# Kernel tuning notes

Hardware: AMD Instinct MI355X
Metric: run time of the kernel (lower is better)

Reference implementation:

```python
import jax, jax.numpy as jnp
import numpy as np

NCE_T = 0.07
TOP_K_RATIO = 0.5
BOTTOM_K_RATIO = 0.1


def setup_inputs() -> dict:
    key = jax.random.key(0)
    k1, k2 = jax.random.split(key)
    N, D = 8192, 256
    feat_q = jax.random.normal(k1, (N, D), dtype=jnp.float32)
    feat_k = jax.random.normal(k2, (N, D), dtype=jnp.float32)
    return {"feat_q": feat_q, "feat_k": feat_k}


def reference(feat_q, feat_k):
    # 2D path of RankNCELoss.forward: feat_q, feat_k are [N, D]
    N = feat_q.shape[0]
    feat_k = jax.lax.stop_gradient(feat_k)  # feat_k.detach()

    # l_pos: per-row dot product  [N, 1]
    l_pos = jnp.sum(feat_q * feat_k, axis=-1, keepdims=True)

    # full similarity matrix [N, N]
    sim = feat_q @ feat_k.T

    # mask diagonal (positives) with -inf
    eye = jnp.eye(N, dtype=bool)
    sim_masked = jnp.where(eye, -jnp.inf, sim)

    # descending sort per row (negate + ascending argsort)
    order = jnp.argsort(-sim_masked, axis=1)               # sorted_indices
    sorted_sim = jnp.take_along_axis(sim_masked, order, axis=1)

    num_neg = N - 1
    k_top = max(1, int(num_neg * TOP_K_RATIO))
    k_bottom = max(0, int(num_neg * BOTTOM_K_RATIO))

    ranks = jnp.arange(N)
    rank_ok = (ranks >= k_bottom) & (ranks < k_top)        # [N]
    select_mask = rank_ok[None, :] & (sorted_sim > -jnp.inf)

    vals = jnp.where(select_mask, sorted_sim, jnp.float32(-10.0))
    rows = jnp.arange(N)[:, None]
    l_neg = jnp.full((N, N), -10.0, dtype=feat_q.dtype).at[rows, order].set(vals)

    out = jnp.concatenate([l_pos, l_neg], axis=1) / NCE_T  # [N, N+1]
    # CrossEntropyLoss(reduction='none') with target 0
    loss = -jax.nn.log_softmax(out, axis=-1)[:, 0]
    return loss
```

## Files before the change

### kernel.cpp

```cpp
#include <hip/hip_runtime.h>
#include <hip/hip_bf16.h>

#define NROW 8192
#define NDIM 256
#define INV_T (1.0f / 0.07f)
#define K_BOT 819
#define K_TOP 4095
#define N_SEL 3276
#define N_UNSEL 4916

typedef unsigned int u32;
typedef unsigned short u16;
typedef short s16;
typedef unsigned long long u64;
typedef __bf16 bf16_t;
typedef s16 s16x8 __attribute__((ext_vector_type(8)));
typedef float f32x4 __attribute__((ext_vector_type(4)));

__device__ __forceinline__ u16 bfbits(float f) {
    return __builtin_bit_cast(u16, (bf16_t)f);
}
__device__ __forceinline__ u16 map16(u16 b) {
    return (b & 0x8000u) ? (u16)~b : (u16)(b | 0x8000u);
}
__device__ __forceinline__ float unmap16(u32 m) {
    u16 b = (m & 0x8000u) ? (u16)(m & 0x7FFFu) : (u16)~(u16)m;
    return __uint_as_float(((u32)b) << 16);
}

__device__ __forceinline__ void gload16(const void* g, void* l) {
    __builtin_amdgcn_global_load_lds(
        (const __attribute__((address_space(1))) u32*)g,
        (__attribute__((address_space(3))) u32*)l, 16, 0, 0);
}

__global__ __launch_bounds__(256) void cvt_bf16(const float* __restrict__ in0,
                                                const float* __restrict__ in1,
                                                u16* __restrict__ out0,
                                                u16* __restrict__ out1) {
    int b = blockIdx.x;
    const float* in = (b < 2048) ? in0 : in1;
    u16* out = (b < 2048) ? out0 : out1;
    int i = ((b & 2047) * 256 + threadIdx.x) * 4;
    float4 v = *(const float4*)(in + i);
    ushort4 o;
    o.x = bfbits(v.x); o.y = bfbits(v.y); o.z = bfbits(v.z); o.w = bfbits(v.w);
    *(ushort4*)(out + i) = o;
}

__global__ __launch_bounds__(512) void gemm_keys(const u16* __restrict__ Qb,
                                                 const u16* __restrict__ Kb,
                                                 u16* __restrict__ Cp) {
    constexpr int BK = 64;
    __shared__ __align__(16) char smem[128 * 132 * 2];
    u16* sA = (u16*)smem;
    u16* sB = (u16*)(smem + 128 * BK * 2);
    u16* sC = (u16*)smem;

    const int tid  = threadIdx.x;
    const int lane = tid & 63;
    const int wid  = tid >> 6;
    const int wr = wid & 1;
    const int wc = wid >> 1;
    const int bm = blockIdx.y * 128;
    const int bn = blockIdx.x * 128;
    const int kg = lane >> 4;
    const int fr = lane & 15;

    const int srr = lane >> 3;
    const int srj = (lane & 7) ^ srr;

    f32x4 acc[4][2] = {};

    for (int k0 = 0; k0 < NDIM; k0 += BK) {
        __syncthreads();
#pragma unroll
        for (int s = 0; s < 2; ++s) {
            int seg = wid * 2 + s;
            int row = seg * 8 + srr;
            gload16(Qb + (size_t)(bm + row) * NDIM + k0 + srj * 8, &sA[seg * 512]);
            gload16(Kb + (size_t)(bn + row) * NDIM + k0 + srj * 8, &sB[seg * 512]);
        }
        __syncthreads();

#pragma unroll
        for (int kk = 0; kk < 2; ++kk) {
            s16x8 af[4], bfv[2];
            const int jp = (kk * 4 + kg) ^ (fr & 7);
#pragma unroll
            for (int m = 0; m < 4; ++m) {
                int row = wr * 64 + m * 16 + fr;
                af[m] = *(const s16x8*)(&sA[row * BK + jp * 8]);
            }
#pragma unroll
            for (int n = 0; n < 2; ++n) {
                int row = wc * 32 + n * 16 + fr;
                bfv[n] = *(const s16x8*)(&sB[row * BK + jp * 8]);
            }
#pragma unroll
            for (int m = 0; m < 4; ++m)
#pragma unroll
                for (int n = 0; n < 2; ++n)
                    acc[m][n] = __builtin_amdgcn_mfma_f32_16x16x32_bf16(
                        af[m], bfv[n], acc[m][n], 0, 0, 0);
        }
    }

    __syncthreads();
#pragma unroll
    for (int m = 0; m < 4; ++m)
#pragma unroll
        for (int n = 0; n < 2; ++n)
#pragma unroll
            for (int jj = 0; jj < 4; ++jj) {
                int r = wr * 64 + m * 16 + kg * 4 + jj;
                int c = wc * 32 + n * 16 + fr;
                sC[r * 132 + c] = map16(bfbits(acc[m][n][jj]));
            }
    __syncthreads();
    if (bm == bn) {
        if (tid < 128) sC[tid * 132 + tid] = 0;
        __syncthreads();
    }
#pragma unroll
    for (int it = 0; it < 4; ++it) {
        int idx = it * 512 + tid;
        int row = idx >> 4, col8 = (idx & 15) * 8;
        *(uint4*)(&Cp[(size_t)(bm + row) * NROW + bn + col8]) =
            *(const uint4*)(&sC[row * 132 + col8]);
    }
}

__device__ __forceinline__ u32 wave_sum_u32(u32 x) {
#pragma unroll
    for (int o = 32; o; o >>= 1) x += __shfl_down(x, o);
    return __shfl(x, 0);
}

__device__ __forceinline__ void resolve_slot(const u32* sub, int slot, u32 rem,
                                             int lane, u32* idxOut, u32* gtOut) {
    u32 word = sub[slot * 64 + lane];
    u32 c0 = word & 0xFFFFu, c1 = word >> 16;
    u32 s0 = c0 + c1, suf = s0;
#pragma unroll
    for (int o = 1; o < 64; o <<= 1) {
        u32 v = __shfl_down(suf, o);
        if (lane + o < 64) suf += v;
    }
    u32 TexL = suf - s0;
    u32 f = 0, pk = 0;
    u32 ab0 = TexL + c1;
    if (rem >= ab0 && rem < ab0 + c0) { f = 1; pk = ((u32)(lane * 2) << 16) | ab0; }
    if (rem >= TexL && rem < TexL + c1) { f = 1; pk = ((u32)(lane * 2 + 1) << 16) | TexL; }
    u64 mm = __ballot(f != 0);
    pk = __shfl(pk, (int)(__ffsll((unsigned long long)mm) - 1));
    *idxOut = pk >> 16;
    *gtOut = pk & 0xFFFFu;
}

__device__ u32 bisect_row(const uint4* rp, u32 rank, int lane) {
    u32 lo = 0, hi = 65535;
    while (lo < hi) {
        u32 mid = (lo + hi) >> 1;
        u32 pc = 0;
        for (int i = 0; i < 16; ++i) {
            uint4 v = rp[i * 64 + lane];
            pc += (u32)((v.x & 0xFFFFu) > mid) + (u32)((v.x >> 16) > mid)
                + (u32)((v.y & 0xFFFFu) > mid) + (u32)((v.y >> 16) > mid)
                + (u32)((v.z & 0xFFFFu) > mid) + (u32)((v.z >> 16) > mid)
                + (u32)((v.w & 0xFFFFu) > mid) + (u32)((v.w >> 16) > mid);
        }
        u32 c = wave_sum_u32(pc);
        if (c <= rank) hi = mid; else lo = mid + 1;
    }
    return lo;
}

#define KLO 0xC100u
#define KHI 0xC280u
#define RSPAN 0x180u
#define NSLOT 3

__global__ __launch_bounds__(128, 8) void rank_lse(const u16* __restrict__ Cp,
                                                   const float* __restrict__ fq,
                                                   const float* __restrict__ fk,
                                                   float* __restrict__ loss) {
    __shared__ u32 lds_s[2][NSLOT * 64];
    const int t = threadIdx.x;
    const int w = t >> 6;
    const int lane = t & 63;
    const int row = blockIdx.x * 2 + w;

    u32* sub = lds_s[w];
    const uint4* rp = (const uint4*)(Cp + (size_t)row * NROW);

    if (lane < 48) *(uint4*)&sub[lane * 4] = make_uint4(0, 0, 0, 0);

    float lp;
    {
        float4 q4 = *(const float4*)(fq + (size_t)row * NDIM + lane * 4);
        float4 k4 = *(const float4*)(fk + (size_t)row * NDIM + lane * 4);
        float p = q4.x * k4.x + q4.y * k4.y + q4.z * k4.z + q4.w * k4.w;
#pragma unroll
        for (int o = 32; o; o >>= 1) p += __shfl_down(p, o);
        lp = __shfl(p, 0);
    }

    u32 cntHi = 0;
#pragma unroll 4
    for (int i = 0; i < 16; ++i) {
        uint4 v = rp[i * 64 + lane];
        u32 vv[4] = { v.x, v.y, v.z, v.w };
#pragma unroll
        for (int q = 0; q < 4; ++q) {
#pragma unroll
            for (int hh = 0; hh < 2; ++hh) {
                u32 key = hh ? (vv[q] >> 16) : (vv[q] & 0xFFFFu);
                cntHi += (key >= KHI) ? 1u : 0u;
                u32 d = key - KLO;
                if (d < RSPAN)
                    atomicAdd(&sub[(d >> 7) * 64 + ((key >> 1) & 63u)],
                              (key & 1u) ? 0x10000u : 1u);
            }
        }
    }
    const u32 CH = wave_sum_u32(cntHi);

    u32 T0, T1, T2;
    {
        u32 w0 = sub[lane], w1 = sub[64 + lane], w2 = sub[128 + lane];
        u32 m0 = (w0 & 0xFFFFu) + (w0 >> 16);
        u32 m1 = (w1 & 0xFFFFu) + (w1 >> 16);
        u32 m2 = (w2 & 0xFFFFu) + (w2 >> 16);
        u32 p01 = wave_sum_u32(m0 | (m1 << 16));
        T2 = wave_sum_u32(m2);
        T0 = p01 & 0xFFFFu; T1 = p01 >> 16;
    }
    const u32 NR = T0 + T1 + T2;

    bool fb = !((CH <= (u32)K_BOT) && ((u32)K_BOT < CH + NR))
            || ((u32)(K_TOP - 1) < CH + NR);

    u32 ua = 0, Ga = 0, Ea = 0;
    float a = 0.f;
    int sA = 0;
    if (!fb) {
        const u32 AT2 = CH, AT1 = CH + T2, AT0 = AT1 + T1;
        u32 ATA;
        if ((u32)K_BOT >= AT0)      { sA = 0; ATA = AT0; }
        else if ((u32)K_BOT >= AT1) { sA = 1; ATA = AT1; }
        else                        { sA = 2; ATA = AT2; }
        const u32 remA = (u32)K_BOT - ATA;
        u32 idxA, gtA;
        resolve_slot(sub, sA, remA, lane, &idxA, &gtA);
        ua = KLO + ((u32)sA << 7) + idxA;
        Ga = ATA + gtA;
        {
            u32 wv = sub[sA * 64 + (idxA >> 1)];
            Ea = (idxA & 1u) ? (wv >> 16) : (wv & 0xFFFFu);
        }
        a = unmap16(ua);
        if (!(a >= 10.9f)) fb = true;
    }

    if (!fb) {
        const float m_ = fmaxf(fmaxf(lp, a), -10.0f) * INV_T;
        float sm = 0.f;
#pragma unroll
        for (int s = 0; s < NSLOT; ++s) {
            u32 wv = sub[s * 64 + lane];
            u32 c0 = wv & 0xFFFFu, c1 = wv >> 16;
            u32 k0 = KLO + ((u32)s << 7) + (u32)(lane * 2);
            u32 k1 = k0 | 1u;
            if (c0 && k0 < ua) sm += (float)c0 * __expf(unmap16(k0) * INV_T - m_);
            if (c1 && k1 < ua) sm += (float)c1 * __expf(unmap16(k1) * INV_T - m_);
        }
#pragma unroll
        for (int o = 32; o; o >>= 1) sm += __shfl_down(sm, o);
        if (lane == 0) {
            float expA = __expf(a * INV_T - m_);
            float tot = sm + (float)(int)(Ga + Ea - (u32)K_BOT) * expA;
            tot += __expf(lp * INV_T - m_)
                 + (float)N_UNSEL * __expf(-10.0f * INV_T - m_);
            loss[row] = m_ + __logf(tot) - lp * INV_T;
        }
    } else {
        u32 fua = bisect_row(rp, (u32)K_BOT, lane);
        u32 fub = bisect_row(rp, (u32)(K_TOP - 1), lane);
        float fa = unmap16(fua);
        const float m_ = fmaxf(fmaxf(lp, fa), -10.0f) * INV_T;
        u32 cga = 0, cea = 0, cgb = 0;
        float sm = 0.f;
        for (int i = 0; i < 16; ++i) {
            uint4 v = rp[i * 64 + lane];
            u32 vv[4] = { v.x, v.y, v.z, v.w };
#pragma unroll
            for (int q = 0; q < 4; ++q) {
#pragma unroll
                for (int hh = 0; hh < 2; ++hh) {
                    u32 u = hh ? (vv[q] >> 16) : (vv[q] & 0xFFFFu);
                    cga += (u > fua); cea += (u == fua); cgb += (u > fub);
                    if (u > fub && u < fua)
                        sm += __expf(unmap16(u) * INV_T - m_);
                }
            }
        }
        u32 fGa = wave_sum_u32(cga), fEa = wave_sum_u32(cea), fGb = wave_sum_u32(cgb);
#pragma unroll
        for (int o = 32; o; o >>= 1) sm += __shfl_down(sm, o);
        if (lane == 0) {
            float bv = unmap16(fub);
            float expA = __expf(fa * INV_T - m_);
            float tot;
            if (fua == fub) {
                tot = (float)N_SEL * expA;
            } else {
                float expB = __expf(bv * INV_T - m_);
                tot = sm + (float)(int)(fGa + fEa - (u32)K_BOT) * expA
                         + (float)(int)((u32)K_TOP - fGb) * expB;
            }
            tot += __expf(lp * INV_T - m_)
                 + (float)N_UNSEL * __expf(-10.0f * INV_T - m_);
            loss[row] = m_ + __logf(tot) - lp * INV_T;
        }
    }
}

extern "C" void kernel_launch(void* const* d_in, const int* in_sizes, int n_in,
                              void* d_out, int out_size, void* d_ws, size_t ws_size,
                              hipStream_t stream) {
    const float* fq = (const float*)d_in[0];
    const float* fk = (const float*)d_in[1];
    float* out = (float*)d_out;

    char* ws = (char*)d_ws;
    u16* keys = (u16*)ws;
    u16* qb = (u16*)(ws + (size_t)NROW * NROW * 2);
    u16* kb = qb + (size_t)NROW * NDIM;

    cvt_bf16<<<4096, 256, 0, stream>>>(fq, fk, qb, kb);
    gemm_keys<<<dim3(NROW / 128, NROW / 128), 512, 0, stream>>>(qb, kb, keys);
    rank_lse<<<NROW / 2, 128, 0, stream>>>(keys, fq, fk, out);
}
```

Measured before the change: 95.97 us.

## Fuse similarity GEMM with per-row histogram ranking, add fallback fixup kernel

```diff
diff --git a/kernel.cpp b/kernel.cpp
--- a/kernel.cpp
+++ b/kernel.cpp
@@ -8,6 +8,9 @@
 #define K_TOP 4095
 #define N_SEL 3276
 #define N_UNSEL 4916
+#define KLO 0xC100u
+#define KHI 0xC280u
+#define RSPAN 0x180u
 
 typedef unsigned int u32;
 typedef unsigned short u16;
@@ -27,11 +30,41 @@
     u16 b = (m & 0x8000u) ? (u16)(m & 0x7FFFu) : (u16)~(u16)m;
     return __uint_as_float(((u32)b) << 16);
 }
+__device__ __forceinline__ float bf2f(s16 v) {
+    return __uint_as_float(((u32)(u16)v) << 16);
+}
 
 __device__ __forceinline__ void gload16(const void* g, void* l) {
     __builtin_amdgcn_global_load_lds(
         (const __attribute__((address_space(1))) u32*)g,
         (__attribute__((address_space(3))) u32*)l, 16, 0, 0);
+}
+
+__device__ __forceinline__ u32 wave_sum_u32(u32 x) {
+#pragma unroll
+    for (int o = 32; o; o >>= 1) x += __shfl_down(x, o);
+    return __shfl(x, 0);
+}
+
+__device__ __forceinline__ void resolve_slot(const u32* sub, int slot, u32 rem,
+                                             int lane, u32* idxOut, u32* gtOut) {
+    u32 word = sub[slot * 64 + lane];
+    u32 c0 = word & 0xFFFFu, c1 = word >> 16;
+    u32 s0 = c0 + c1, suf = s0;
+#pragma unroll
+    for (int o = 1; o < 64; o <<= 1) {
+        u32 v = __shfl_down(suf, o);
+        if (lane + o < 64) suf += v;
+    }
+    u32 TexL = suf - s0;
+    u32 f = 0, pk = 0;
+    u32 ab0 = TexL + c1;
+    if (rem >= ab0 && rem < ab0 + c0) { f = 1; pk = ((u32)(lane * 2) << 16) | ab0; }
+    if (rem >= TexL && rem < TexL + c1) { f = 1; pk = ((u32)(lane * 2 + 1) << 16) | TexL; }
+    u64 mm = __ballot(f != 0);
+    pk = __shfl(pk, (int)(__ffsll((unsigned long long)mm) - 1));
+    *idxOut = pk >> 16;
+    *gtOut = pk & 0xFFFFu;
 }
 
 __global__ __launch_bounds__(256) void cvt_bf16(const float* __restrict__ in0,
@@ -48,276 +81,257 @@
     *(ushort4*)(out + i) = o;
 }
 
-__global__ __launch_bounds__(512) void gemm_keys(const u16* __restrict__ Qb,
-                                                 const u16* __restrict__ Kb,
-                                                 u16* __restrict__ Cp) {
-    constexpr int BK = 64;
-    __shared__ __align__(16) char smem[128 * 132 * 2];
-    u16* sA = (u16*)smem;
-    u16* sB = (u16*)(smem + 128 * BK * 2);
-    u16* sC = (u16*)smem;
+__global__ __launch_bounds__(512) void fused_rank(const u16* __restrict__ Qb,
+                                                  const u16* __restrict__ Kb,
+                                                  const float* __restrict__ fq,
+                                                  const float* __restrict__ fk,
+                                                  float* __restrict__ loss,
+                                                  u32* __restrict__ flags) {
+    __shared__ __align__(16) u16 sA[32 * 256];
+    __shared__ __align__(16) u16 sB[2][128 * 128];
+    __shared__ u32 hist[32 * 192];
+    __shared__ u32 cntHiRow[32];
 
     const int tid  = threadIdx.x;
     const int lane = tid & 63;
     const int wid  = tid >> 6;
-    const int wr = wid & 1;
-    const int wc = wid >> 1;
-    const int bm = blockIdx.y * 128;
-    const int bn = blockIdx.x * 128;
-    const int kg = lane >> 4;
-    const int fr = lane & 15;
-
-    const int srr = lane >> 3;
-    const int srj = (lane & 7) ^ srr;
-
-    f32x4 acc[4][2] = {};
-
-    for (int k0 = 0; k0 < NDIM; k0 += BK) {
+    const int kg   = lane >> 4;
+    const int fr   = lane & 15;
+    const int r0   = blockIdx.x * 32;
+
+    for (int i = tid; i < 32 * 192; i += 512) hist[i] = 0;
+    if (tid < 32) cntHiRow[tid] = 0;
+
+#pragma unroll
+    for (int s = 0; s < 2; ++s) {
+        int seg = wid * 2 + s;
+        int c = seg * 64 + lane;
+        int row = c >> 5, jp = c & 31;
+        int j = jp ^ (row & 7);
+        gload16(Qb + (size_t)(r0 + row) * NDIM + j * 8, &sA[seg * 512]);
+    }
+
+    auto STAGE = [&](int buf, int step) {
+        int h2 = step & 1, ct2 = step >> 1;
+        u16* dst = &sB[buf][0];
+#pragma unroll
+        for (int s2 = 0; s2 < 4; ++s2) {
+            int seg = wid * 4 + s2;
+            int c = seg * 64 + lane;
+            int row = c >> 4, jp = c & 15;
+            int j = jp ^ (row & 7);
+            gload16(Kb + (size_t)(ct2 * 128 + row) * NDIM + h2 * 128 + j * 8,
+                    dst + seg * 512);
+        }
+    };
+
+    STAGE(0, 0);
+    __syncthreads();
+
+    f32x4 acc[2] = {};
+    u32 cntHi[2][4] = {};
+
+    for (int s = 0; s < 128; ++s) {
+        const int buf = s & 1;
+        if (s + 1 < 128) STAGE(buf ^ 1, s + 1);
+        const int h = s & 1, ct = s >> 1;
+#pragma unroll
+        for (int ks = 0; ks < 4; ++ks) {
+            s16x8 bv = *(const s16x8*)&sB[buf][(wid * 16 + fr) * 128 +
+                                              (((ks * 4 + kg) ^ (fr & 7)) * 8)];
+#pragma unroll
+            for (int m = 0; m < 2; ++m) {
+                s16x8 av = *(const s16x8*)&sA[(m * 16 + fr) * 256 +
+                                              (((h * 16 + ks * 4 + kg) ^ (fr & 7)) * 8)];
+                acc[m] = __builtin_amdgcn_mfma_f32_16x16x32_bf16(av, bv, acc[m], 0, 0, 0);
+            }
+        }
+        if (h == 1) {
+            const int gcol = ct * 128 + wid * 16 + fr;
+#pragma unroll
+            for (int m = 0; m < 2; ++m) {
+#pragma unroll
+                for (int jj = 0; jj < 4; ++jj) {
+                    int rowLocal = m * 16 + kg * 4 + jj;
+                    u32 key = (u32)map16(bfbits(acc[m][jj]));
+                    if (r0 + rowLocal != gcol) {
+                        cntHi[m][jj] += (key >= KHI) ? 1u : 0u;
+                        u32 d = key - KLO;
+                        if (d < RSPAN)
+                            atomicAdd(&hist[rowLocal * 192 + (int)(d >> 7) * 64 +
+                                            (int)((key >> 1) & 63u)],
+                                      (key & 1u) ? 0x10000u : 1u);
+                    }
+                }
+                acc[m][0] = 0.f; acc[m][1] = 0.f; acc[m][2] = 0.f; acc[m][3] = 0.f;
+            }
+        }
         __syncthreads();
-#pragma unroll
-        for (int s = 0; s < 2; ++s) {
-            int seg = wid * 2 + s;
-            int row = seg * 8 + srr;
-            gload16(Qb + (size_t)(bm + row) * NDIM + k0 + srj * 8, &sA[seg * 512]);
-            gload16(Kb + (size_t)(bn + row) * NDIM + k0 + srj * 8, &sB[seg * 512]);
-        }
-        __syncthreads();
-
-#pragma unroll
-        for (int kk = 0; kk < 2; ++kk) {
-            s16x8 af[4], bfv[2];
-            const int jp = (kk * 4 + kg) ^ (fr & 7);
-#pragma unroll
-            for (int m = 0; m < 4; ++m) {
-                int row = wr * 64 + m * 16 + fr;
-                af[m] = *(const s16x8*)(&sA[row * BK + jp * 8]);
-            }
-#pragma unroll
-            for (int n = 0; n < 2; ++n) {
-                int row = wc * 32 + n * 16 + fr;
-                bfv[n] = *(const s16x8*)(&sB[row * BK + jp * 8]);
-            }
-#pragma unroll
-            for (int m = 0; m < 4; ++m)
-#pragma unroll
-                for (int n = 0; n < 2; ++n)
-                    acc[m][n] = __builtin_amdgcn_mfma_f32_16x16x32_bf16(
-                        af[m], bfv[n], acc[m][n], 0, 0, 0);
-        }
-    }
-
+    }
+
+#pragma unroll
+    for (int m = 0; m < 2; ++m)
+#pragma unroll
+        for (int jj = 0; jj < 4; ++jj) {
+            u32 v = cntHi[m][jj];
+            v += __shfl_down(v, 8, 16);
+            v += __shfl_down(v, 4, 16);
+            v += __shfl_down(v, 2, 16);
+            v += __shfl_down(v, 1, 16);
+            if (fr == 0) atomicAdd(&cntHiRow[m * 16 + kg * 4 + jj], v);
+        }
     __syncthreads();
-#pragma unroll
-    for (int m = 0; m < 4; ++m)
-#pragma unroll
-        for (int n = 0; n < 2; ++n)
-#pragma unroll
-            for (int jj = 0; jj < 4; ++jj) {
-                int r = wr * 64 + m * 16 + kg * 4 + jj;
-                int c = wc * 32 + n * 16 + fr;
-                sC[r * 132 + c] = map16(bfbits(acc[m][n][jj]));
-            }
-    __syncthreads();
-    if (bm == bn) {
-        if (tid < 128) sC[tid * 132 + tid] = 0;
-        __syncthreads();
-    }
-#pragma unroll
-    for (int it = 0; it < 4; ++it) {
-        int idx = it * 512 + tid;
-        int row = idx >> 4, col8 = (idx & 15) * 8;
-        *(uint4*)(&Cp[(size_t)(bm + row) * NROW + bn + col8]) =
-            *(const uint4*)(&sC[row * 132 + col8]);
-    }
-}
-
-__device__ __forceinline__ u32 wave_sum_u32(u32 x) {
-#pragma unroll
-    for (int o = 32; o; o >>= 1) x += __shfl_down(x, o);
-    return __shfl(x, 0);
-}
-
-__device__ __forceinline__ void resolve_slot(const u32* sub, int slot, u32 rem,
-                                             int lane, u32* idxOut, u32* gtOut) {
-    u32 word = sub[slot * 64 + lane];
-    u32 c0 = word & 0xFFFFu, c1 = word >> 16;
-    u32 s0 = c0 + c1, suf = s0;
-#pragma unroll
-    for (int o = 1; o < 64; o <<= 1) {
-        u32 v = __shfl_down(suf, o);
-        if (lane + o < 64) suf += v;
-    }
-    u32 TexL = suf - s0;
-    u32 f = 0, pk = 0;
-    u32 ab0 = TexL + c1;
-    if (rem >= ab0 && rem < ab0 + c0) { f = 1; pk = ((u32)(lane * 2) << 16) | ab0; }
-    if (rem >= TexL && rem < TexL + c1) { f = 1; pk = ((u32)(lane * 2 + 1) << 16) | TexL; }
-    u64 mm = __ballot(f != 0);
-    pk = __shfl(pk, (int)(__ffsll((unsigned long long)mm) - 1));
-    *idxOut = pk >> 16;
-    *gtOut = pk & 0xFFFFu;
-}
-
-__device__ u32 bisect_row(const uint4* rp, u32 rank, int lane) {
-    u32 lo = 0, hi = 65535;
-    while (lo < hi) {
-        u32 mid = (lo + hi) >> 1;
-        u32 pc = 0;
-        for (int i = 0; i < 16; ++i) {
-            uint4 v = rp[i * 64 + lane];
-            pc += (u32)((v.x & 0xFFFFu) > mid) + (u32)((v.x >> 16) > mid)
-                + (u32)((v.y & 0xFFFFu) > mid) + (u32)((v.y >> 16) > mid)
-                + (u32)((v.z & 0xFFFFu) > mid) + (u32)((v.z >> 16) > mid)
-                + (u32)((v.w & 0xFFFFu) > mid) + (u32)((v.w >> 16) > mid);
-        }
-        u32 c = wave_sum_u32(pc);
-        if (c <= rank) hi = mid; else lo = mid + 1;
-    }
-    return lo;
-}
-
-#define KLO 0xC100u
-#define KHI 0xC280u
-#define RSPAN 0x180u
-#define NSLOT 3
-
-__global__ __launch_bounds__(128, 8) void rank_lse(const u16* __restrict__ Cp,
-                                                   const float* __restrict__ fq,
-                                                   const float* __restrict__ fk,
-                                                   float* __restrict__ loss) {
-    __shared__ u32 lds_s[2][NSLOT * 64];
-    const int t = threadIdx.x;
-    const int w = t >> 6;
-    const int lane = t & 63;
-    const int row = blockIdx.x * 2 + w;
-
-    u32* sub = lds_s[w];
-    const uint4* rp = (const uint4*)(Cp + (size_t)row * NROW);
-
-    if (lane < 48) *(uint4*)&sub[lane * 4] = make_uint4(0, 0, 0, 0);
-
-    float lp;
-    {
-        float4 q4 = *(const float4*)(fq + (size_t)row * NDIM + lane * 4);
-        float4 k4 = *(const float4*)(fk + (size_t)row * NDIM + lane * 4);
-        float p = q4.x * k4.x + q4.y * k4.y + q4.z * k4.z + q4.w * k4.w;
-#pragma unroll
-        for (int o = 32; o; o >>= 1) p += __shfl_down(p, o);
-        lp = __shfl(p, 0);
-    }
-
-    u32 cntHi = 0;
-#pragma unroll 4
-    for (int i = 0; i < 16; ++i) {
-        uint4 v = rp[i * 64 + lane];
-        u32 vv[4] = { v.x, v.y, v.z, v.w };
-#pragma unroll
-        for (int q = 0; q < 4; ++q) {
-#pragma unroll
-            for (int hh = 0; hh < 2; ++hh) {
-                u32 key = hh ? (vv[q] >> 16) : (vv[q] & 0xFFFFu);
-                cntHi += (key >= KHI) ? 1u : 0u;
-                u32 d = key - KLO;
-                if (d < RSPAN)
-                    atomicAdd(&sub[(d >> 7) * 64 + ((key >> 1) & 63u)],
-                              (key & 1u) ? 0x10000u : 1u);
-            }
-        }
-    }
-    const u32 CH = wave_sum_u32(cntHi);
-
-    u32 T0, T1, T2;
-    {
-        u32 w0 = sub[lane], w1 = sub[64 + lane], w2 = sub[128 + lane];
-        u32 m0 = (w0 & 0xFFFFu) + (w0 >> 16);
-        u32 m1 = (w1 & 0xFFFFu) + (w1 >> 16);
-        u32 m2 = (w2 & 0xFFFFu) + (w2 >> 16);
-        u32 p01 = wave_sum_u32(m0 | (m1 << 16));
-        T2 = wave_sum_u32(m2);
-        T0 = p01 & 0xFFFFu; T1 = p01 >> 16;
-    }
-    const u32 NR = T0 + T1 + T2;
-
-    bool fb = !((CH <= (u32)K_BOT) && ((u32)K_BOT < CH + NR))
-            || ((u32)(K_TOP - 1) < CH + NR);
-
-    u32 ua = 0, Ga = 0, Ea = 0;
-    float a = 0.f;
-    int sA = 0;
-    if (!fb) {
-        const u32 AT2 = CH, AT1 = CH + T2, AT0 = AT1 + T1;
-        u32 ATA;
-        if ((u32)K_BOT >= AT0)      { sA = 0; ATA = AT0; }
-        else if ((u32)K_BOT >= AT1) { sA = 1; ATA = AT1; }
-        else                        { sA = 2; ATA = AT2; }
-        const u32 remA = (u32)K_BOT - ATA;
-        u32 idxA, gtA;
-        resolve_slot(sub, sA, remA, lane, &idxA, &gtA);
-        ua = KLO + ((u32)sA << 7) + idxA;
-        Ga = ATA + gtA;
+
+    for (int rr = 0; rr < 4; ++rr) {
+        const int rowLocal = rr * 8 + wid;
+        const int grow = r0 + rowLocal;
+        const u32* sub = &hist[rowLocal * 192];
+
+        float lp;
         {
-            u32 wv = sub[sA * 64 + (idxA >> 1)];
-            Ea = (idxA & 1u) ? (wv >> 16) : (wv & 0xFFFFu);
-        }
-        a = unmap16(ua);
-        if (!(a >= 10.9f)) fb = true;
-    }
-
-    if (!fb) {
+            float4 q4 = *(const float4*)(fq + (size_t)grow * NDIM + lane * 4);
+            float4 k4 = *(const float4*)(fk + (size_t)grow * NDIM + lane * 4);
+            float p = q4.x * k4.x + q4.y * k4.y + q4.z * k4.z + q4.w * k4.w;
+#pragma unroll
+            for (int o = 32; o; o >>= 1) p += __shfl_down(p, o);
+            lp = __shfl(p, 0);
+        }
+        const u32 CH = cntHiRow[rowLocal];
+
+        u32 T0, T1, T2;
+        {
+            u32 w0 = sub[lane], w1 = sub[64 + lane], w2 = sub[128 + lane];
+            u32 m0 = (w0 & 0xFFFFu) + (w0 >> 16);
+            u32 m1 = (w1 & 0xFFFFu) + (w1 >> 16);
+            u32 m2 = (w2 & 0xFFFFu) + (w2 >> 16);
+            u32 p01 = wave_sum_u32(m0 | (m1 << 16));
+            T2 = wave_sum_u32(m2);
+            T0 = p01 & 0xFFFFu; T1 = p01 >> 16;
+        }
+        const u32 NR = T0 + T1 + T2;
+
+        bool fb = !((CH <= (u32)K_BOT) && ((u32)K_BOT < CH + NR))
+                || ((u32)(K_TOP - 1) < CH + NR);
+
+        u32 ua = 0, Ga = 0, Ea = 0;
+        float a = 0.f;
+        if (!fb) {
+            const u32 AT2 = CH, AT1 = CH + T2, AT0 = AT1 + T1;
+            int sA_;
+            u32 ATA;
+            if ((u32)K_BOT >= AT0)      { sA_ = 0; ATA = AT0; }
+            else if ((u32)K_BOT >= AT1) { sA_ = 1; ATA = AT1; }
+            else                        { sA_ = 2; ATA = AT2; }
+            const u32 remA = (u32)K_BOT - ATA;
+            u32 idxA, gtA;
+            resolve_slot(sub, sA_, remA, lane, &idxA, &gtA);
+            ua = KLO + ((u32)sA_ << 7) + idxA;
+            Ga = ATA + gtA;
+            {
+                u32 wv = sub[sA_ * 64 + (idxA >> 1)];
+                Ea = (idxA & 1u) ? (wv >> 16) : (wv & 0xFFFFu);
+            }
+            a = unmap16(ua);
+            if (!(a >= 10.9f)) fb = true;
+        }
+
+        if (!fb) {
+            const float m_ = fmaxf(fmaxf(lp, a), -10.0f) * INV_T;
+            float sm = 0.f;
+#pragma unroll
+            for (int ss = 0; ss < 3; ++ss) {
+                u32 wv = sub[ss * 64 + lane];
+                u32 c0 = wv & 0xFFFFu, c1 = wv >> 16;
+                u32 k0 = KLO + ((u32)ss << 7) + (u32)(lane * 2);
+                u32 k1 = k0 | 1u;
+                if (c0 && k0 < ua) sm += (float)c0 * __expf(unmap16(k0) * INV_T - m_);
+                if (c1 && k1 < ua) sm += (float)c1 * __expf(unmap16(k1) * INV_T - m_);
+            }
+#pragma unroll
+            for (int o = 32; o; o >>= 1) sm += __shfl_down(sm, o);
+            if (lane == 0) {
+                float expA = __expf(a * INV_T - m_);
+                float tot = sm + (float)(int)(Ga + Ea - (u32)K_BOT) * expA;
+                tot += __expf(lp * INV_T - m_)
+                     + (float)N_UNSEL * __expf(-10.0f * INV_T - m_);
+                loss[grow] = m_ + __logf(tot) - lp * INV_T;
+                flags[grow] = 0u;
+            }
+        } else {
+            if (lane == 0) flags[grow] = 1u;
+        }
+    }
+}
+
+__global__ __launch_bounds__(256) void fixup(const u16* __restrict__ Qb,
+                                             const u16* __restrict__ Kb,
+                                             const float* __restrict__ fq,
+                                             const float* __restrict__ fk,
+                                             const u32* __restrict__ flags,
+                                             float* __restrict__ loss) {
+    __shared__ u16 skey[4][NROW];
+    const int wid = threadIdx.x >> 6, lane = threadIdx.x & 63;
+    const int gw = blockIdx.x * 4 + wid;
+
+    for (int rr = 0; rr < 32; ++rr) {
+        const int row = gw * 32 + rr;
+        if (!flags[row]) continue;
+        u16* K = skey[wid];
+        for (int j = 0; j < 128; ++j) {
+            int c = j * 64 + lane;
+            float dot = 0.f;
+            for (int kc = 0; kc < 32; ++kc) {
+                s16x8 qv = *(const s16x8*)(Qb + (size_t)row * NDIM + kc * 8);
+                s16x8 kv = *(const s16x8*)(Kb + (size_t)c * NDIM + kc * 8);
+#pragma unroll
+                for (int e = 0; e < 8; ++e) dot += bf2f(qv[e]) * bf2f(kv[e]);
+            }
+            K[c] = (c == row) ? (u16)0 : map16(bfbits(dot));
+        }
+        auto cntAbove = [&](u32 mid) {
+            u32 pc = 0;
+            for (int i = 0; i < 128; ++i) pc += (u32)(K[i * 64 + lane] > mid);
+            return wave_sum_u32(pc);
+        };
+        u32 lo = 0, hi = 65535;
+        while (lo < hi) { u32 mid = (lo + hi) >> 1;
+            if (cntAbove(mid) <= (u32)K_BOT) hi = mid; else lo = mid + 1; }
+        const u32 ua = lo;
+        lo = 0; hi = 65535;
+        while (lo < hi) { u32 mid = (lo + hi) >> 1;
+            if (cntAbove(mid) <= (u32)(K_TOP - 1)) hi = mid; else lo = mid + 1; }
+        const u32 ub = lo;
+        float lp;
+        {
+            float4 q4 = *(const float4*)(fq + (size_t)row * NDIM + lane * 4);
+            float4 k4 = *(const float4*)(fk + (size_t)row * NDIM + lane * 4);
+            float p = q4.x * k4.x + q4.y * k4.y + q4.z * k4.z + q4.w * k4.w;
+#pragma unroll
+            for (int o = 32; o; o >>= 1) p += __shfl_down(p, o);
+            lp = __shfl(p, 0);
+        }
+        const float a = unmap16(ua);
         const float m_ = fmaxf(fmaxf(lp, a), -10.0f) * INV_T;
+        u32 cga = 0, cea = 0, cgb = 0;
         float sm = 0.f;
-#pragma unroll
-        for (int s = 0; s < NSLOT; ++s) {
-            u32 wv = sub[s * 64 + lane];
-            u32 c0 = wv & 0xFFFFu, c1 = wv >> 16;
-            u32 k0 = KLO + ((u32)s << 7) + (u32)(lane * 2);
-            u32 k1 = k0 | 1u;
-            if (c0 && k0 < ua) sm += (float)c0 * __expf(unmap16(k0) * INV_T - m_);
-            if (c1 && k1 < ua) sm += (float)c1 * __expf(unmap16(k1) * INV_T - m_);
-        }
+        for (int i = 0; i < 128; ++i) {
+            u32 u = K[i * 64 + lane];
+            cga += (u > ua); cea += (u == ua); cgb += (u > ub);
+            if (u > ub && u < ua) sm += __expf(unmap16(u) * INV_T - m_);
+        }
+        u32 Ga = wave_sum_u32(cga), Ea = wave_sum_u32(cea), Gb = wave_sum_u32(cgb);
 #pragma unroll
         for (int o = 32; o; o >>= 1) sm += __shfl_down(sm, o);
         if (lane == 0) {
+            float bv = unmap16(ub);
             float expA = __expf(a * INV_T - m_);
-            float tot = sm + (float)(int)(Ga + Ea - (u32)K_BOT) * expA;
-            tot += __expf(lp * INV_T - m_)
-                 + (float)N_UNSEL * __expf(-10.0f * INV_T - m_);
-            loss[row] = m_ + __logf(tot) - lp * INV_T;
-        }
-    } else {
-        u32 fua = bisect_row(rp, (u32)K_BOT, lane);
-        u32 fub = bisect_row(rp, (u32)(K_TOP - 1), lane);
-        float fa = unmap16(fua);
-        const float m_ = fmaxf(fmaxf(lp, fa), -10.0f) * INV_T;
-        u32 cga = 0, cea = 0, cgb = 0;
-        float sm = 0.f;
-        for (int i = 0; i < 16; ++i) {
-            uint4 v = rp[i * 64 + lane];
-            u32 vv[4] = { v.x, v.y, v.z, v.w };
-#pragma unroll
-            for (int q = 0; q < 4; ++q) {
-#pragma unroll
-                for (int hh = 0; hh < 2; ++hh) {
-                    u32 u = hh ? (vv[q] >> 16) : (vv[q] & 0xFFFFu);
-                    cga += (u > fua); cea += (u == fua); cgb += (u > fub);
-                    if (u > fub && u < fua)
-                        sm += __expf(unmap16(u) * INV_T - m_);
-                }
-            }
-        }
-        u32 fGa = wave_sum_u32(cga), fEa = wave_sum_u32(cea), fGb = wave_sum_u32(cgb);
-#pragma unroll
-        for (int o = 32; o; o >>= 1) sm += __shfl_down(sm, o);
-        if (lane == 0) {
-            float bv = unmap16(fub);
-            float expA = __expf(fa * INV_T - m_);
             float tot;
-            if (fua == fub) {
+            if (ua == ub) {
                 tot = (float)N_SEL * expA;
             } else {
                 float expB = __expf(bv * INV_T - m_);
-                tot = sm + (float)(int)(fGa + fEa - (u32)K_BOT) * expA
-                         + (float)(int)((u32)K_TOP - fGb) * expB;
+                tot = sm + (float)(int)(Ga + Ea - (u32)K_BOT) * expA
+                         + (float)(int)((u32)K_TOP - Gb) * expB;
             }
             tot += __expf(lp * INV_T - m_)
                  + (float)N_UNSEL * __expf(-10.0f * INV_T - m_);
@@ -334,11 +348,11 @@
     float* out = (float*)d_out;
 
     char* ws = (char*)d_ws;
-    u16* keys = (u16*)ws;
-    u16* qb = (u16*)(ws + (size_t)NROW * NROW * 2);
+    u16* qb = (u16*)ws;
     u16* kb = qb + (size_t)NROW * NDIM;
+    u32* flags = (u32*)(ws + 2 * (size_t)NROW * NDIM * 2);
 
     cvt_bf16<<<4096, 256, 0, stream>>>(fq, fk, qb, kb);
-    gemm_keys<<<dim3(NROW / 128, NROW / 128), 512, 0, stream>>>(qb, kb, keys);
-    rank_lse<<<NROW / 2, 128, 0, stream>>>(keys, fq, fk, out);
-}
+    fused_rank<<<256, 512, 0, stream>>>(qb, kb, fq, fk, out, flags);
+    fixup<<<64, 256, 0, stream>>>(qb, kb, fq, fk, flags, out);
+}
```

Result: slower. 194.1 us (+102.2%).
